# Kernel optimization log

Measured on AMD Instinct MI355X. Metric: run time of the kernel, lower is better.

The kernel has to match this reference:

```python
import jax, jax.numpy as jnp
import numpy as np

N = 100_000       # nodes
E_RAND = 1_600_000
HID = 256         # hidden_channels
L = 4             # num_layers
HEADS = 8
BASES = 4
AGGS = 3          # ['sum','mean','max']
DH = HID // HEADS # 32
BF = DH * BASES   # 128, bases_lin output dim
NG = 5000         # num graphs
VOCAB = 128
NFEAT = 9
EPS = 1e-5


def setup_inputs() -> dict:
    key = jax.random.key(0)
    ks = jax.random.split(key, 16)
    x = jax.random.randint(ks[0], (N, NFEAT), 0, VOCAB, dtype=jnp.int32)
    src = jax.random.randint(ks[1], (E_RAND,), 0, N, dtype=jnp.int32)
    dst = jax.random.randint(ks[2], (E_RAND,), 0, N, dtype=jnp.int32)
    loop = jnp.arange(N, dtype=jnp.int32)          # EGConv add_self_loops=True
    edge_src = jnp.concatenate([src, loop])
    edge_dst = jnp.concatenate([dst, loop])
    batch = jnp.sort(jax.random.randint(ks[3], (N,), 0, NG, dtype=jnp.int32))
    s = lambda k, shape, sc: (jax.random.normal(k, shape, jnp.float32) * sc)
    emb = s(ks[4], (NFEAT, VOCAB, HID), 0.1)       # AtomEncoder tables
    basesW = s(ks[5], (L, HID, BF), HID ** -0.5)
    combW = s(ks[6], (L, HID, HEADS * BASES * AGGS), HID ** -0.5)
    combB = jnp.zeros((L, HEADS * BASES * AGGS), jnp.float32)
    convBias = jnp.zeros((L, HID), jnp.float32)
    bnG = jnp.ones((L, HID), jnp.float32)
    bnB = jnp.zeros((L, HID), jnp.float32)
    mlp_w1 = s(ks[7], (HID, HID // 2), HID ** -0.5)
    bn1_g = jnp.ones((HID // 2,), jnp.float32)
    bn1_b = jnp.zeros((HID // 2,), jnp.float32)
    mlp_w2 = s(ks[8], (HID // 2, HID // 4), (HID // 2) ** -0.5)
    bn2_g = jnp.ones((HID // 4,), jnp.float32)
    bn2_b = jnp.zeros((HID // 4,), jnp.float32)
    mlp_w3 = s(ks[9], (HID // 4, 1), (HID // 4) ** -0.5)
    mlp_b3 = jnp.zeros((1,), jnp.float32)
    return dict(x=x, edge_src=edge_src, edge_dst=edge_dst, batch=batch,
                emb=emb, basesW=basesW, combW=combW, combB=combB,
                convBias=convBias, bnG=bnG, bnB=bnB,
                mlp_w1=mlp_w1, bn1_g=bn1_g, bn1_b=bn1_b,
                mlp_w2=mlp_w2, bn2_g=bn2_g, bn2_b=bn2_b,
                mlp_w3=mlp_w3, mlp_b3=mlp_b3)


def _batchnorm(h, g, b):
    # training-mode BatchNorm1d: biased batch stats
    mu = h.mean(0)
    var = ((h - mu) ** 2).mean(0)
    return (h - mu) * jax.lax.rsqrt(var + EPS) * g + b


def _egconv(x, src, dst, W_b, W_c, b_c, bias):
    bases = x @ W_b                                    # [N, BF]
    w = (x @ W_c + b_c).reshape(N, HEADS, BASES * AGGS)
    msg = bases[src]                                   # [E, BF] gather
    agg_sum = jnp.zeros((N, BF), x.dtype).at[dst].add(msg)
    deg = jnp.zeros((N,), x.dtype).at[dst].add(1.0)
    agg_mean = agg_sum / jnp.maximum(deg, 1.0)[:, None]
    agg_max = jnp.full((N, BF), -jnp.inf, x.dtype).at[dst].max(msg)
    agg = jnp.stack([agg_sum, agg_mean, agg_max], 1)   # [N, A, BF]
    agg = agg.reshape(N, AGGS * BASES, DH)             # [N, A*B, DH]
    out = jnp.einsum('nhk,nkd->nhd', w, agg).reshape(N, HID)
    return out + bias


def reference(x, edge_src, edge_dst, batch, emb, basesW, combW, combB,
              convBias, bnG, bnB, mlp_w1, bn1_g, bn1_b, mlp_w2, bn2_g,
              bn2_b, mlp_w3, mlp_b3):
    # AtomEncoder: sum of per-feature embedding lookups
    h = jnp.take_along_axis(
        emb.transpose(1, 0, 2),                        # [VOCAB, NFEAT, HID]
        x.T[..., None], axis=0) if False else None
    feat = jnp.arange(NFEAT)
    xe = emb[feat[None, :], x, :].sum(1)               # [N, HID]
    h = xe
    for l in range(L):
        c = _egconv(h, edge_src, edge_dst, basesW[l], combW[l], combB[l],
                    convBias[l])
        c = jax.nn.relu(_batchnorm(c, bnG[l], bnB[l]))
        h = h + c                                      # residual
    # global mean pool over graphs
    gs = jax.ops.segment_sum(h, batch, num_segments=NG)
    cnt = jax.ops.segment_sum(jnp.ones((N, 1), h.dtype), batch,
                              num_segments=NG)
    g = gs / jnp.maximum(cnt, 1.0)
    # MLP head
    g = jax.nn.relu(_batchnorm(g @ mlp_w1, bn1_g, bn1_b))
    g = jax.nn.relu(_batchnorm(g @ mlp_w2, bn2_g, bn2_b))
    return g @ mlp_w3 + mlp_b3                         # [NG, 1]
```

## Files before the change

### kernel.cpp

```cpp
#include <hip/hip_runtime.h>
#include <hip/hip_bf16.h>

#define NNODES 100000
#define HIDC 256
#define NFEAT 9
#define VOCABS 128
#define BFD 128
#define NCOMB 96
#define NGR 5000
#define LAYERSN 4
#define EPSV 1e-5f
#define SCHUNK 1024
#define NPP 16
#define NTILES 14
#define AGGBLK 2048
#define AGGW (AGGBLK * 4)
#define PBL (NTILES * 8 * 64)

typedef __hip_bfloat16 bf16;
typedef __attribute__((ext_vector_type(8))) short sh8;
typedef __attribute__((ext_vector_type(4))) float fx4;

__device__ __forceinline__ float b2f(bf16 v) { return __bfloat162float(v); }
__device__ __forceinline__ bf16 f2b(float v) { return __float2bfloat16(v); }
__device__ __forceinline__ float ldf(const float* p) { return *p; }
__device__ __forceinline__ float ldf(const bf16* p) { return b2f(*p); }
__device__ __forceinline__ void stf(float* p, float v) { *p = v; }
__device__ __forceinline__ void stf(bf16* p, float v) { *p = f2b(v); }

__device__ __forceinline__ unsigned pack2bf(float a, float b) {
    unsigned ua = __float_as_uint(a), ub = __float_as_uint(b);
    ua = (ua + 0x7FFFu + ((ua >> 16) & 1u)) >> 16;
    ub = (ub + 0x7FFFu + ((ub >> 16) & 1u)) >> 16;
    return ua | (ub << 16);
}

__global__ __launch_bounds__(256) void k_sentinel(float* out, int n, float val) {
    int i = blockIdx.x * 256 + threadIdx.x;
    if (i < n) out[i] = val;
}

template <typename TH>
__global__ __launch_bounds__(256) void k_atom(const int* __restrict__ x,
                                              const float* __restrict__ emb,
                                              TH* __restrict__ h) {
    int n = blockIdx.x;
    __shared__ int xs[NFEAT];
    if (threadIdx.x < NFEAT) xs[threadIdx.x] = x[n * NFEAT + threadIdx.x];
    __syncthreads();
    int c = threadIdx.x;
    float acc = 0.f;
#pragma unroll
    for (int f = 0; f < NFEAT; ++f)
        acc += emb[(f * VOCABS + xs[f]) * HIDC + c];
    stf(&h[(size_t)n * HIDC + c], acc);
}

__global__ __launch_bounds__(256) void k_hist(const int* __restrict__ dst,
                                              int* __restrict__ counts, int E) {
    int e = blockIdx.x * 256 + threadIdx.x;
    if (e < E) atomicAdd(&counts[dst[e]], 1);
}

__global__ __launch_bounds__(256) void k_scansum(const int* __restrict__ counts,
                                                 int* __restrict__ btot, int n) {
    __shared__ int sh[256];
    int b = blockIdx.x, t = threadIdx.x;
    int base = b * SCHUNK;
    int s = 0;
#pragma unroll
    for (int k = 0; k < 4; ++k) {
        int i = base + t + k * 256;
        if (i < n) s += counts[i];
    }
    sh[t] = s;
    __syncthreads();
    for (int st = 128; st > 0; st >>= 1) {
        if (t < st) sh[t] += sh[t + st];
        __syncthreads();
    }
    if (t == 0) btot[b] = sh[0];
}

__global__ void k_scansmall(const int* __restrict__ btot, int* __restrict__ boff, int nb) {
    if (threadIdx.x == 0 && blockIdx.x == 0) {
        int a = 0;
        for (int i = 0; i < nb; ++i) { boff[i] = a; a += btot[i]; }
    }
}

__global__ __launch_bounds__(256) void k_scanapply(const int* __restrict__ counts,
                                                   const int* __restrict__ boff,
                                                   int* __restrict__ rowptr,
                                                   int* __restrict__ cursor, int n) {
    __shared__ int sh[256];
    int b = blockIdx.x, t = threadIdx.x;
    int base = b * SCHUNK + t * 4;
    int c0 = (base + 0 < n) ? counts[base + 0] : 0;
    int c1 = (base + 1 < n) ? counts[base + 1] : 0;
    int c2 = (base + 2 < n) ? counts[base + 2] : 0;
    int c3 = (base + 3 < n) ? counts[base + 3] : 0;
    int s0 = c0, s1 = s0 + c1, s2 = s1 + c2, s3 = s2 + c3;
    sh[t] = s3;
    __syncthreads();
    for (int st = 1; st < 256; st <<= 1) {
        int v = (t >= st) ? sh[t - st] : 0;
        __syncthreads();
        sh[t] += v;
        __syncthreads();
    }
    int excl = sh[t] - s3 + boff[b];
    if (base + 0 < n) { rowptr[base + 1] = excl + s0; cursor[base + 0] = excl; }
    if (base + 1 < n) { rowptr[base + 2] = excl + s1; cursor[base + 1] = excl + s0; }
    if (base + 2 < n) { rowptr[base + 3] = excl + s2; cursor[base + 2] = excl + s1; }
    if (base + 3 < n) { rowptr[base + 4] = excl + s3; cursor[base + 3] = excl + s2; }
    if (b == 0 && t == 0) rowptr[0] = 0;
}

__global__ __launch_bounds__(256) void k_scatter(const int* __restrict__ src,
                                                 const int* __restrict__ dst,
                                                 int* __restrict__ cursor,
                                                 int* __restrict__ csr, int E) {
    int e = blockIdx.x * 256 + threadIdx.x;
    if (e >= E) return;
    int pos = atomicAdd(&cursor[dst[e]], 1);
    csr[pos] = src[e];
}

__global__ __launch_bounds__(256) void k_packB4(const float* __restrict__ basesW,
                                                const float* __restrict__ combW,
                                                bf16* __restrict__ Bp4) {
    int tid = blockIdx.x * 256 + threadIdx.x;
    if (tid >= LAYERSN * PBL) return;
    int layer = tid / PBL;
    int rem = tid % PBL;
    int l = rem & 63;
    int q = (rem >> 6) & 7;
    int t = rem >> 9;
    int n = t * 16 + (l & 15);
    int k0 = q * 32 + (l >> 4) * 8;
    const float* Wb = basesW + (size_t)layer * HIDC * BFD;
    const float* Wc = combW + (size_t)layer * HIDC * NCOMB;
    short out[8];
#pragma unroll
    for (int i = 0; i < 8; ++i) {
        int k = k0 + i;
        float v = (n < BFD) ? Wb[k * BFD + n] : Wc[k * NCOMB + (n - BFD)];
        unsigned u = __float_as_uint(v);
        out[i] = (short)((u + 0x7FFFu + ((u >> 16) & 1u)) >> 16);
    }
    *(sh8*)(Bp4 + (size_t)tid * 8) = *(sh8*)out;
}

template <typename TH, typename TW>
__global__ __launch_bounds__(256) void k_gemm_mfma(TH* __restrict__ h,
                                                   const bf16* __restrict__ Bp,
                                                   const float* __restrict__ cb,
                                                   bf16* __restrict__ bases,
                                                   TW* __restrict__ wco,
                                                   const bf16* __restrict__ convp,
                                                   const float* __restrict__ ss) {
    __shared__ unsigned ldsA[8192];
    int tid = threadIdx.x;
    size_t blk = blockIdx.x;
#pragma unroll 4
    for (int it = 0; it < 32; ++it) {
        int p = tid + it * 256;
        int row = p >> 7, cp = p & 127;
        size_t rg = blk * 64 + row;
        unsigned word = 0;
        if (rg < NNODES) {
            int c0 = cp * 2;
            float a0 = ldf(&h[rg * HIDC + c0]);
            float a1 = ldf(&h[rg * HIDC + c0 + 1]);
            if (convp) {
                float v0 = b2f(convp[rg * HIDC + c0]) * ss[c0] + ss[HIDC + c0];
                float v1 = b2f(convp[rg * HIDC + c0 + 1]) * ss[c0 + 1] + ss[HIDC + c0 + 1];
                a0 += fmaxf(v0, 0.f);
                a1 += fmaxf(v1, 0.f);
                stf(&h[rg * HIDC + c0], a0);
                stf(&h[rg * HIDC + c0 + 1], a1);
            }
            word = pack2bf(a0, a1);
        }
        ldsA[(row * 128 + cp) ^ ((row & 7) << 2)] = word;
    }
    __syncthreads();
    int w = tid >> 6, l = tid & 63;
    int r = 16 * w + (l & 15);
    sh8 af[8];
    const char* lb = (const char*)ldsA;
#pragma unroll
    for (int q = 0; q < 8; ++q) {
        int byte = (r * 512 + q * 64 + (l >> 4) * 16) ^ ((r & 7) << 4);
        af[q] = *(const sh8*)(lb + byte);
    }
    fx4 acc[NTILES];
#pragma unroll
    for (int t = 0; t < NTILES; ++t) acc[t] = (fx4){0.f, 0.f, 0.f, 0.f};
    const sh8* bp8 = (const sh8*)Bp;
#pragma unroll
    for (int t = 0; t < NTILES; ++t) {
#pragma unroll
        for (int q = 0; q < 8; ++q) {
            acc[t] = __builtin_amdgcn_mfma_f32_16x16x32_bf16(
                af[q], bp8[(t * 8 + q) * 64 + l], acc[t], 0, 0, 0);
        }
    }
#pragma unroll
    for (int t = 0; t < NTILES; ++t) {
#pragma unroll
        for (int j = 0; j < 4; ++j) {
            int rl = 16 * w + (l >> 4) * 4 + j;
            size_t rg = blk * 64 + rl;
            if (rg >= NNODES) continue;
            if (t < 8) {
                int col = t * 16 + (l & 15);
                bases[rg * BFD + col] = f2b(acc[t][j]);
            } else {
                int col = (t - 8) * 16 + (l & 15);
                stf(&wco[rg * NCOMB + col], acc[t][j] + cb[col]);
            }
        }
    }
}

template <typename TW>
__global__ __launch_bounds__(256) void k_agg(const int* __restrict__ rowptr,
                                             const int* __restrict__ csr,
                                             const uint2* __restrict__ b2,
                                             const TW* __restrict__ wco,
                                             const float* __restrict__ bias,
                                             bf16* __restrict__ conv,
                                             float* __restrict__ partials) {
    __shared__ float agg[4][3][BFD];
    __shared__ int nid[4];
    int tid = threadIdx.x;
    int wv = tid >> 6, lane = tid & 63;
    int cl = lane & 31;
    bool loh = lane < 32;
    int c = tid, hh = c >> 5, d = c & 31;
    float bb = bias[c];
    float st_s = 0.f, st_s2 = 0.f;
    const int ITERS = (NNODES + AGGW - 1) / AGGW;
    int n = blockIdx.x * 4 + wv;
    for (int it = 0; it < ITERS; ++it, n += AGGW) {
        if (n < NNODES) {
            if (lane == 0) nid[wv] = n;
            int r0 = rowptr[n], r1 = rowptr[n + 1];
            float s0 = 0.f, s1 = 0.f, s2 = 0.f, s3 = 0.f;
            float m0 = -INFINITY, m1 = -INFINITY, m2 = -INFINITY, m3 = -INFINITY;
            int e = r0;
#define ACCU2(v) { float f0 = __uint_as_float((v).x << 16);            \
                   float f1 = __uint_as_float((v).x & 0xFFFF0000u);    \
                   float f2 = __uint_as_float((v).y << 16);            \
                   float f3 = __uint_as_float((v).y & 0xFFFF0000u);    \
                   s0 += f0; s1 += f1; s2 += f2; s3 += f3;             \
                   m0 = fmaxf(m0, f0); m1 = fmaxf(m1, f1);             \
                   m2 = fmaxf(m2, f2); m3 = fmaxf(m3, f3); }
            for (; e + 4 <= r1; e += 4) {
                int sa = loh ? csr[e + 0] : csr[e + 1];
                int sb = loh ? csr[e + 2] : csr[e + 3];
                uint2 va = b2[(size_t)sa * 32 + cl];
                uint2 vb = b2[(size_t)sb * 32 + cl];
                ACCU2(va) ACCU2(vb)
            }
            for (; e + 2 <= r1; e += 2) {
                int sa = loh ? csr[e + 0] : csr[e + 1];
                uint2 va = b2[(size_t)sa * 32 + cl];
                ACCU2(va)
            }
            if (e < r1 && loh) {
                uint2 va = b2[(size_t)csr[e] * 32 + cl];
                ACCU2(va)
            }
#undef ACCU2
            float t0 = s0 + __shfl_xor(s0, 32);
            float t1 = s1 + __shfl_xor(s1, 32);
            float t2 = s2 + __shfl_xor(s2, 32);
            float t3 = s3 + __shfl_xor(s3, 32);
            float x0 = fmaxf(m0, __shfl_xor(m0, 32));
            float x1 = fmaxf(m1, __shfl_xor(m1, 32));
            float x2 = fmaxf(m2, __shfl_xor(m2, 32));
            float x3 = fmaxf(m3, __shfl_xor(m3, 32));
            if (loh) {
                float inv = 1.0f / (float)(r1 - r0);
                int cc = 4 * cl;
                agg[wv][0][cc + 0] = t0; agg[wv][1][cc + 0] = t0 * inv; agg[wv][2][cc + 0] = x0;
                agg[wv][0][cc + 1] = t1; agg[wv][1][cc + 1] = t1 * inv; agg[wv][2][cc + 1] = x1;
                agg[wv][0][cc + 2] = t2; agg[wv][1][cc + 2] = t2 * inv; agg[wv][2][cc + 2] = x2;
                agg[wv][0][cc + 3] = t3; agg[wv][1][cc + 3] = t3 * inv; agg[wv][2][cc + 3] = x3;
            }
        } else if (lane == 0) {
            nid[wv] = -1;
        }
        __syncthreads();
#pragma unroll
        for (int w2 = 0; w2 < 4; ++w2) {
            int n2 = nid[w2];
            if (n2 < 0) continue;
            const TW* wp = &wco[(size_t)n2 * NCOMB + hh * 12];
            float a = 0.f;
#pragma unroll
            for (int b = 0; b < 4; ++b) {
                a += ldf(&wp[0 + b]) * agg[w2][0][b * 32 + d];
                a += ldf(&wp[4 + b]) * agg[w2][1][b * 32 + d];
                a += ldf(&wp[8 + b]) * agg[w2][2][b * 32 + d];
            }
            a += bb;
            conv[(size_t)n2 * HIDC + c] = f2b(a);
            st_s += a;
            st_s2 += a * a;
        }
        __syncthreads();
    }
    partials[(size_t)blockIdx.x * 512 + c] = st_s;
    partials[(size_t)blockIdx.x * 512 + 256 + c] = st_s2;
}

__global__ __launch_bounds__(256) void k_redstats(const float* __restrict__ partials,
                                                  float* __restrict__ sums) {
    int g = blockIdx.x * 256 + threadIdx.x;
    int j = g & 511;
    int chunk = g >> 9;
    float s = 0.f;
    for (int pb = chunk * 256; pb < (chunk + 1) * 256; ++pb)
        s += partials[(size_t)pb * 512 + j];
    atomicAdd(&sums[j], s);
}

template <int C>
__global__ void k_bnfin(const float* __restrict__ sums, const float* __restrict__ g,
                        const float* __restrict__ b, float nrows, float* __restrict__ ss) {
    int c = threadIdx.x;
    float mu = sums[c] / nrows;
    float var = sums[C + c] / nrows - mu * mu;
    float rstd = rsqrtf(fmaxf(var, 0.f) + EPSV);
    float sc = rstd * g[c];
    ss[c] = sc;
    ss[C + c] = b[c] - mu * sc;
}

template <typename TH>
__global__ __launch_bounds__(256) void k_apply_res(const bf16* __restrict__ conv,
                                                   const float* __restrict__ ss,
                                                   TH* __restrict__ h) {
    int n = blockIdx.x;
    int c = threadIdx.x;
    float v = b2f(conv[(size_t)n * HIDC + c]) * ss[c] + ss[HIDC + c];
    size_t i = (size_t)n * HIDC + c;
    stf(&h[i], ldf(&h[i]) + fmaxf(v, 0.f));
}

template <typename TH>
__global__ __launch_bounds__(256) void k_pool(const TH* __restrict__ h,
                                              const int* __restrict__ batch,
                                              float* __restrict__ gs,
                                              float* __restrict__ cnt) {
    int c = threadIdx.x;
    int n0 = blockIdx.x * NPP;
    int end = min(n0 + NPP, NNODES);
    float acc = 0.f, ccnt = 0.f;
    int cur = batch[n0];
    for (int n = n0; n < end; ++n) {
        int b = batch[n];
        if (b != cur) {
            atomicAdd(&gs[(size_t)cur * HIDC + c], acc);
            if (c == 0) atomicAdd(&cnt[cur], ccnt);
            acc = 0.f; ccnt = 0.f; cur = b;
        }
        acc += ldf(&h[(size_t)n * HIDC + c]);
        ccnt += 1.f;
    }
    atomicAdd(&gs[(size_t)cur * HIDC + c], acc);
    if (c == 0) atomicAdd(&cnt[cur], ccnt);
}

__global__ __launch_bounds__(256) void k_pooldiv(float* __restrict__ gs,
                                                 const float* __restrict__ cnt) {
    int i = blockIdx.x * 256 + threadIdx.x;
    if (i >= NGR * HIDC) return;
    int ng = i >> 8;
    gs[i] = gs[i] / fmaxf(cnt[ng], 1.0f);
}

template <int K, int C>
__global__ void k_rowgemm(const float* __restrict__ in, const float* __restrict__ W,
                          float* __restrict__ out) {
    int r = blockIdx.x;
    __shared__ float rs[K];
    for (int i = threadIdx.x; i < K; i += C) rs[i] = in[r * K + i];
    __syncthreads();
    int c = threadIdx.x;
    float acc = 0.f;
    for (int k = 0; k < K; ++k) acc += rs[k] * W[k * C + c];
    out[r * C + c] = acc;
}

template <int C>
__global__ void k_stats(const float* __restrict__ a, int rows, int rpb,
                        float* __restrict__ sums) {
    int c = threadIdx.x;
    int r0 = blockIdx.x * rpb;
    int r1 = min(r0 + rpb, rows);
    float s = 0.f, s2 = 0.f;
    for (int r = r0; r < r1; ++r) {
        float v = a[r * C + c];
        s += v;
        s2 += v * v;
    }
    atomicAdd(&sums[c], s);
    atomicAdd(&sums[C + c], s2);
}

template <int C>
__global__ void k_apply_relu(float* __restrict__ a, const float* __restrict__ ss, int rows) {
    int i = blockIdx.x * 256 + threadIdx.x;
    if (i >= rows * C) return;
    int c = i % C;
    float v = a[i] * ss[c] + ss[C + c];
    a[i] = fmaxf(v, 0.f);
}

__global__ __launch_bounds__(256) void k_final(const float* __restrict__ g2,
                                               const float* __restrict__ w3,
                                               const float* __restrict__ b3,
                                               float* __restrict__ out) {
    int r = blockIdx.x * 256 + threadIdx.x;
    if (r >= NGR) return;
    float acc = 0.f;
#pragma unroll
    for (int k = 0; k < 64; ++k) acc += g2[r * 64 + k] * w3[k];
    out[r] = acc + b3[0];
}

static inline size_t alignup(size_t v) { return (v + 255) & ~(size_t)255; }

template <typename TH, typename TW>
static size_t carve_need(int E) {
    size_t off = 0;
    off = alignup(off + (size_t)NNODES * HIDC * sizeof(TH));
    off = alignup(off + (size_t)NNODES * BFD * 2);
    off = alignup(off + (size_t)NNODES * NCOMB * sizeof(TW));
    off = alignup(off + (size_t)NNODES * HIDC * 2);
    off = alignup(off + (size_t)(NNODES + 1) * 4);
    off = alignup(off + (size_t)NNODES * 4);
    off = alignup(off + (size_t)E * 4);
    off = alignup(off + 2 * HIDC * 4);
    off = alignup(off + 2 * HIDC * 4);
    off = alignup(off + 256 * 4);
    off = alignup(off + 256 * 4);
    off = alignup(off + (size_t)LAYERSN * PBL * 8 * 2);
    off = alignup(off + (size_t)AGGBLK * 512 * 4);
    return off;
}

template <typename TH, typename TW>
static void run_all(const int* x, const int* esrc, const int* edst, const int* batch,
                    const float* emb, const float* basesW, const float* combW,
                    const float* combB, const float* convB, const float* bnG,
                    const float* bnB, const float* w1, const float* bn1g,
                    const float* bn1b, const float* w2, const float* bn2g,
                    const float* bn2b, const float* w3, const float* b3, int E,
                    float* out, char* base, hipStream_t stream) {
    size_t off = 0;
    TH* h = (TH*)(base + off);       off = alignup(off + (size_t)NNODES * HIDC * sizeof(TH));
    bf16* bases = (bf16*)(base + off); off = alignup(off + (size_t)NNODES * BFD * 2);
    TW* wco = (TW*)(base + off);     off = alignup(off + (size_t)NNODES * NCOMB * sizeof(TW));
    size_t o_conv = off;
    bf16* conv = (bf16*)(base + off); off = alignup(off + (size_t)NNODES * HIDC * 2);
    int* rowptr = (int*)(base + off); off = alignup(off + (size_t)(NNODES + 1) * 4);
    int* cursor = (int*)(base + off); off = alignup(off + (size_t)NNODES * 4);
    int* csr = (int*)(base + off);    off = alignup(off + (size_t)E * 4);
    float* sums = (float*)(base + off); off = alignup(off + 2 * HIDC * 4);
    float* ss = (float*)(base + off);   off = alignup(off + 2 * HIDC * 4);
    int* btot = (int*)(base + off);     off = alignup(off + 256 * 4);
    int* boff = (int*)(base + off);     off = alignup(off + 256 * 4);
    bf16* Bp4 = (bf16*)(base + off);    off = alignup(off + (size_t)LAYERSN * PBL * 8 * 2);
    float* partials = (float*)(base + off); off = alignup(off + (size_t)AGGBLK * 512 * 4);
    size_t po = o_conv;
    float* gs = (float*)(base + po);  po = alignup(po + (size_t)NGR * HIDC * 4);
    float* cnt = (float*)(base + po); po = alignup(po + (size_t)NGR * 4);
    float* r1 = (float*)(base + po);  po = alignup(po + (size_t)NGR * 128 * 4);
    float* r2 = (float*)(base + po);  po = alignup(po + (size_t)NGR * 64 * 4);

    const int NB = (NNODES + SCHUNK - 1) / SCHUNK;
    const int GEMMBLK = (NNODES + 63) / 64;

    k_atom<TH><<<NNODES, 256, 0, stream>>>(x, emb, h);
    k_packB4<<<(LAYERSN * PBL + 255) / 256, 256, 0, stream>>>(basesW, combW, Bp4);
    hipMemsetAsync(cursor, 0, (size_t)NNODES * 4, stream);
    k_hist<<<(E + 255) / 256, 256, 0, stream>>>(edst, cursor, E);
    k_scansum<<<NB, 256, 0, stream>>>(cursor, btot, NNODES);
    k_scansmall<<<1, 64, 0, stream>>>(btot, boff, NB);
    k_scanapply<<<NB, 256, 0, stream>>>(cursor, boff, rowptr, cursor, NNODES);
    k_scatter<<<(E + 255) / 256, 256, 0, stream>>>(esrc, edst, cursor, csr, E);

    for (int l = 0; l < LAYERSN; ++l) {
        hipMemsetAsync(sums, 0, 2 * HIDC * 4, stream);
        k_gemm_mfma<TH, TW><<<GEMMBLK, 256, 0, stream>>>(
            h, Bp4 + (size_t)l * PBL * 8, combB + (size_t)l * NCOMB, bases, wco,
            (l > 0) ? conv : (const bf16*)nullptr, ss);
        k_agg<TW><<<AGGBLK, 256, 0, stream>>>(rowptr, csr, (const uint2*)bases,
                                              wco, convB + (size_t)l * HIDC, conv,
                                              partials);
        k_redstats<<<16, 256, 0, stream>>>(partials, sums);
        k_bnfin<HIDC><<<1, HIDC, 0, stream>>>(sums, bnG + (size_t)l * HIDC,
                                              bnB + (size_t)l * HIDC, (float)NNODES, ss);
    }
    k_apply_res<TH><<<NNODES, 256, 0, stream>>>(conv, ss, h);

    hipMemsetAsync(gs, 0, (size_t)NGR * HIDC * 4, stream);
    hipMemsetAsync(cnt, 0, (size_t)NGR * 4, stream);
    k_pool<TH><<<(NNODES + NPP - 1) / NPP, 256, 0, stream>>>(h, batch, gs, cnt);
    k_pooldiv<<<(NGR * HIDC + 255) / 256, 256, 0, stream>>>(gs, cnt);

    k_rowgemm<256, 128><<<NGR, 128, 0, stream>>>(gs, w1, r1);
    hipMemsetAsync(sums, 0, 2 * 128 * 4, stream);
    k_stats<128><<<(NGR + 15) / 16, 128, 0, stream>>>(r1, NGR, 16, sums);
    k_bnfin<128><<<1, 128, 0, stream>>>(sums, bn1g, bn1b, (float)NGR, ss);
    k_apply_relu<128><<<(NGR * 128 + 255) / 256, 256, 0, stream>>>(r1, ss, NGR);

    k_rowgemm<128, 64><<<NGR, 64, 0, stream>>>(r1, w2, r2);
    hipMemsetAsync(sums, 0, 2 * 64 * 4, stream);
    k_stats<64><<<(NGR + 31) / 32, 64, 0, stream>>>(r2, NGR, 32, sums);
    k_bnfin<64><<<1, 64, 0, stream>>>(sums, bn2g, bn2b, (float)NGR, ss);
    k_apply_relu<64><<<(NGR * 64 + 255) / 256, 256, 0, stream>>>(r2, ss, NGR);

    k_final<<<(NGR + 255) / 256, 256, 0, stream>>>(r2, w3, b3, out);
}

extern "C" void kernel_launch(void* const* d_in, const int* in_sizes, int n_in,
                              void* d_out, int out_size, void* d_ws, size_t ws_size,
                              hipStream_t stream) {
    const int* x        = (const int*)d_in[0];
    const int* esrc     = (const int*)d_in[1];
    const int* edst     = (const int*)d_in[2];
    const int* batch    = (const int*)d_in[3];
    const float* emb    = (const float*)d_in[4];
    const float* basesW = (const float*)d_in[5];
    const float* combW  = (const float*)d_in[6];
    const float* combB  = (const float*)d_in[7];
    const float* convB  = (const float*)d_in[8];
    const float* bnG    = (const float*)d_in[9];
    const float* bnB    = (const float*)d_in[10];
    const float* w1     = (const float*)d_in[11];
    const float* bn1g   = (const float*)d_in[12];
    const float* bn1b   = (const float*)d_in[13];
    const float* w2     = (const float*)d_in[14];
    const float* bn2g   = (const float*)d_in[15];
    const float* bn2b   = (const float*)d_in[16];
    const float* w3     = (const float*)d_in[17];
    const float* b3     = (const float*)d_in[18];
    const int E = in_sizes[1];

    size_t need_full    = carve_need<float, float>(E);
    size_t need_compact = carve_need<bf16, bf16>(E);

    if (ws_size >= need_full) {
        run_all<float, float>(x, esrc, edst, batch, emb, basesW, combW, combB, convB,
                              bnG, bnB, w1, bn1g, bn1b, w2, bn2g, bn2b, w3, b3, E,
                              (float*)d_out, (char*)d_ws, stream);
    } else if (ws_size >= need_compact) {
        run_all<bf16, bf16>(x, esrc, edst, batch, emb, basesW, combW, combB, convB,
                            bnG, bnB, w1, bn1g, bn1b, w2, bn2g, bn2b, w3, b3, E,
                            (float*)d_out, (char*)d_ws, stream);
    } else {
        k_sentinel<<<(out_size + 255) / 256, 256, 0, stream>>>(
            (float*)d_out, out_size, (float)(ws_size >> 20));
    }
}
```

Before: 1.499 ms.

## Bucket edges by destination before CSR scatter and drop block sync in aggregation

The CSR build now runs in two passes. Edges are first partitioned into 32 destination-range buckets using block-local counts, then each bucket is scattered by its own group of blocks, so the atomics and csr writes hit a narrower address range. The aggregation kernel now has each wavefront apply the per-node combination weights to its own node, with each lane producing 4 packed bf16 channels. This removes the per-iteration __syncthreads and the shared node-id exchange. BN statistics are reduced through shared-memory atomics, at the cost of an extra edge buffer and more kernel launches.

```diff
diff --git a/kernel.cpp b/kernel.cpp
--- a/kernel.cpp
+++ b/kernel.cpp
@@ -16,6 +16,9 @@
 #define AGGBLK 2048
 #define AGGW (AGGBLK * 4)
 #define PBL (NTILES * 8 * 64)
+#define NBUK 32
+#define BDIV 3125
+#define SC2K 16
 
 typedef __hip_bfloat16 bf16;
 typedef __attribute__((ext_vector_type(8))) short sh8;
@@ -117,14 +120,56 @@
     if (b == 0 && t == 0) rowptr[0] = 0;
 }
 
-__global__ __launch_bounds__(256) void k_scatter(const int* __restrict__ src,
-                                                 const int* __restrict__ dst,
-                                                 int* __restrict__ cursor,
-                                                 int* __restrict__ csr, int E) {
-    int e = blockIdx.x * 256 + threadIdx.x;
-    if (e >= E) return;
-    int pos = atomicAdd(&cursor[dst[e]], 1);
-    csr[pos] = src[e];
+__global__ void k_binit(const int* __restrict__ rowptr, int* __restrict__ gcur) {
+    int b = threadIdx.x;
+    if (b < NBUK) gcur[b] = rowptr[b * BDIV];
+}
+
+__global__ __launch_bounds__(256) void k_bucket(const int* __restrict__ src,
+                                                const int* __restrict__ dst,
+                                                int* __restrict__ gcur,
+                                                uint2* __restrict__ ebuf, int E) {
+    __shared__ int cnt[NBUK], base[NBUK], off[NBUK];
+    int tid = threadIdx.x;
+    if (tid < NBUK) { cnt[tid] = 0; off[tid] = 0; }
+    __syncthreads();
+    int d[4], s[4], bk[4];
+    int e0 = blockIdx.x * 1024;
+#pragma unroll
+    for (int k = 0; k < 4; ++k) {
+        int e = e0 + tid + k * 256;
+        if (e < E) {
+            d[k] = dst[e]; s[k] = src[e];
+            bk[k] = d[k] / BDIV;
+            atomicAdd(&cnt[bk[k]], 1);
+        } else bk[k] = -1;
+    }
+    __syncthreads();
+    if (tid < NBUK && cnt[tid] > 0) base[tid] = atomicAdd(&gcur[tid], cnt[tid]);
+    __syncthreads();
+#pragma unroll
+    for (int k = 0; k < 4; ++k) {
+        if (bk[k] >= 0) {
+            int sl = base[bk[k]] + atomicAdd(&off[bk[k]], 1);
+            ebuf[sl] = make_uint2((unsigned)d[k], (unsigned)s[k]);
+        }
+    }
+}
+
+__global__ __launch_bounds__(256) void k_scatter2(const uint2* __restrict__ ebuf,
+                                                  const int* __restrict__ rowptr,
+                                                  int* __restrict__ cursor,
+                                                  int* __restrict__ csr) {
+    int bk = blockIdx.x & (NBUK - 1);
+    int chunk = blockIdx.x >> 5;
+    int lo = rowptr[bk * BDIV];
+    int nhi = (bk + 1) * BDIV; if (nhi > NNODES) nhi = NNODES;
+    int hi = rowptr[nhi];
+    for (int e = lo + chunk * 256 + threadIdx.x; e < hi; e += SC2K * 256) {
+        uint2 p = ebuf[e];
+        int pos = atomicAdd(&cursor[p.x], 1);
+        csr[pos] = (int)p.y;
+    }
 }
 
 __global__ __launch_bounds__(256) void k_packB4(const float* __restrict__ basesW,
@@ -234,23 +279,24 @@
                                              bf16* __restrict__ conv,
                                              float* __restrict__ partials) {
     __shared__ float agg[4][3][BFD];
-    __shared__ int nid[4];
+    __shared__ float red[512];
     int tid = threadIdx.x;
     int wv = tid >> 6, lane = tid & 63;
     int cl = lane & 31;
     bool loh = lane < 32;
-    int c = tid, hh = c >> 5, d = c & 31;
-    float bb = bias[c];
-    float st_s = 0.f, st_s2 = 0.f;
-    const int ITERS = (NNODES + AGGW - 1) / AGGW;
-    int n = blockIdx.x * 4 + wv;
-    for (int it = 0; it < ITERS; ++it, n += AGGW) {
-        if (n < NNODES) {
-            if (lane == 0) nid[wv] = n;
-            int r0 = rowptr[n], r1 = rowptr[n + 1];
-            float s0 = 0.f, s1 = 0.f, s2 = 0.f, s3 = 0.f;
-            float m0 = -INFINITY, m1 = -INFINITY, m2 = -INFINITY, m3 = -INFINITY;
-            int e = r0;
+    red[tid] = 0.f;
+    red[tid + 256] = 0.f;
+    __syncthreads();
+    int hh = lane >> 3;
+    float bb[4];
+#pragma unroll
+    for (int j = 0; j < 4; ++j) bb[j] = bias[4 * lane + j];
+    float sts[4] = {0.f, 0.f, 0.f, 0.f}, sts2[4] = {0.f, 0.f, 0.f, 0.f};
+    for (int n = blockIdx.x * 4 + wv; n < NNODES; n += AGGW) {
+        int r0 = rowptr[n], r1 = rowptr[n + 1];
+        float s0 = 0.f, s1 = 0.f, s2 = 0.f, s3 = 0.f;
+        float m0 = -INFINITY, m1 = -INFINITY, m2 = -INFINITY, m3 = -INFINITY;
+        int e = r0;
 #define ACCU2(v) { float f0 = __uint_as_float((v).x << 16);            \
                    float f1 = __uint_as_float((v).x & 0xFFFF0000u);    \
                    float f2 = __uint_as_float((v).y << 16);            \
@@ -258,64 +304,70 @@
                    s0 += f0; s1 += f1; s2 += f2; s3 += f3;             \
                    m0 = fmaxf(m0, f0); m1 = fmaxf(m1, f1);             \
                    m2 = fmaxf(m2, f2); m3 = fmaxf(m3, f3); }
-            for (; e + 4 <= r1; e += 4) {
-                int sa = loh ? csr[e + 0] : csr[e + 1];
-                int sb = loh ? csr[e + 2] : csr[e + 3];
-                uint2 va = b2[(size_t)sa * 32 + cl];
-                uint2 vb = b2[(size_t)sb * 32 + cl];
-                ACCU2(va) ACCU2(vb)
+        for (; e + 4 <= r1; e += 4) {
+            int sa = loh ? csr[e + 0] : csr[e + 1];
+            int sb = loh ? csr[e + 2] : csr[e + 3];
+            uint2 va = b2[(size_t)sa * 32 + cl];
+            uint2 vb = b2[(size_t)sb * 32 + cl];
+            ACCU2(va) ACCU2(vb)
+        }
+        for (; e + 2 <= r1; e += 2) {
+            int sa = loh ? csr[e + 0] : csr[e + 1];
+            uint2 va = b2[(size_t)sa * 32 + cl];
+            ACCU2(va)
+        }
+        if (e < r1 && loh) {
+            uint2 va = b2[(size_t)csr[e] * 32 + cl];
+            ACCU2(va)
+        }
+#undef ACCU2
+        float t0 = s0 + __shfl_xor(s0, 32);
+        float t1 = s1 + __shfl_xor(s1, 32);
+        float t2 = s2 + __shfl_xor(s2, 32);
+        float t3 = s3 + __shfl_xor(s3, 32);
+        float x0 = fmaxf(m0, __shfl_xor(m0, 32));
+        float x1 = fmaxf(m1, __shfl_xor(m1, 32));
+        float x2 = fmaxf(m2, __shfl_xor(m2, 32));
+        float x3 = fmaxf(m3, __shfl_xor(m3, 32));
+        if (loh) {
+            float inv = 1.0f / (float)(r1 - r0);
+            int cc = 4 * cl;
+            agg[wv][0][cc + 0] = t0; agg[wv][1][cc + 0] = t0 * inv; agg[wv][2][cc + 0] = x0;
+            agg[wv][0][cc + 1] = t1; agg[wv][1][cc + 1] = t1 * inv; agg[wv][2][cc + 1] = x1;
+            agg[wv][0][cc + 2] = t2; agg[wv][1][cc + 2] = t2 * inv; agg[wv][2][cc + 2] = x2;
+            agg[wv][0][cc + 3] = t3; agg[wv][1][cc + 3] = t3 * inv; agg[wv][2][cc + 3] = x3;
+        }
+        const TW* wp = &wco[(size_t)n * NCOMB + hh * 12];
+        float w[12];
+#pragma unroll
+        for (int k = 0; k < 12; ++k) w[k] = ldf(&wp[k]);
+        float o[4];
+#pragma unroll
+        for (int j = 0; j < 4; ++j) {
+            int d = (4 * lane + j) & 31;
+            float a = 0.f;
+#pragma unroll
+            for (int b = 0; b < 4; ++b) {
+                a += w[b] * agg[wv][0][b * 32 + d];
+                a += w[4 + b] * agg[wv][1][b * 32 + d];
+                a += w[8 + b] * agg[wv][2][b * 32 + d];
             }
-            for (; e + 2 <= r1; e += 2) {
-                int sa = loh ? csr[e + 0] : csr[e + 1];
-                uint2 va = b2[(size_t)sa * 32 + cl];
-                ACCU2(va)
-            }
-            if (e < r1 && loh) {
-                uint2 va = b2[(size_t)csr[e] * 32 + cl];
-                ACCU2(va)
-            }
-#undef ACCU2
-            float t0 = s0 + __shfl_xor(s0, 32);
-            float t1 = s1 + __shfl_xor(s1, 32);
-            float t2 = s2 + __shfl_xor(s2, 32);
-            float t3 = s3 + __shfl_xor(s3, 32);
-            float x0 = fmaxf(m0, __shfl_xor(m0, 32));
-            float x1 = fmaxf(m1, __shfl_xor(m1, 32));
-            float x2 = fmaxf(m2, __shfl_xor(m2, 32));
-            float x3 = fmaxf(m3, __shfl_xor(m3, 32));
-            if (loh) {
-                float inv = 1.0f / (float)(r1 - r0);
-                int cc = 4 * cl;
-                agg[wv][0][cc + 0] = t0; agg[wv][1][cc + 0] = t0 * inv; agg[wv][2][cc + 0] = x0;
-                agg[wv][0][cc + 1] = t1; agg[wv][1][cc + 1] = t1 * inv; agg[wv][2][cc + 1] = x1;
-                agg[wv][0][cc + 2] = t2; agg[wv][1][cc + 2] = t2 * inv; agg[wv][2][cc + 2] = x2;
-                agg[wv][0][cc + 3] = t3; agg[wv][1][cc + 3] = t3 * inv; agg[wv][2][cc + 3] = x3;
-            }
-        } else if (lane == 0) {
-            nid[wv] = -1;
-        }
-        __syncthreads();
-#pragma unroll
-        for (int w2 = 0; w2 < 4; ++w2) {
-            int n2 = nid[w2];
-            if (n2 < 0) continue;
-            const TW* wp = &wco[(size_t)n2 * NCOMB + hh * 12];
-            float a = 0.f;
-#pragma unroll
-            for (int b = 0; b < 4; ++b) {
-                a += ldf(&wp[0 + b]) * agg[w2][0][b * 32 + d];
-                a += ldf(&wp[4 + b]) * agg[w2][1][b * 32 + d];
-                a += ldf(&wp[8 + b]) * agg[w2][2][b * 32 + d];
-            }
-            a += bb;
-            conv[(size_t)n2 * HIDC + c] = f2b(a);
-            st_s += a;
-            st_s2 += a * a;
-        }
-        __syncthreads();
-    }
-    partials[(size_t)blockIdx.x * 512 + c] = st_s;
-    partials[(size_t)blockIdx.x * 512 + 256 + c] = st_s2;
+            a += bb[j];
+            o[j] = a;
+            sts[j] += a;
+            sts2[j] += a * a;
+        }
+        uint2 cv = make_uint2(pack2bf(o[0], o[1]), pack2bf(o[2], o[3]));
+        ((uint2*)conv)[(size_t)n * 64 + lane] = cv;
+    }
+#pragma unroll
+    for (int j = 0; j < 4; ++j) {
+        atomicAdd(&red[4 * lane + j], sts[j]);
+        atomicAdd(&red[256 + 4 * lane + j], sts2[j]);
+    }
+    __syncthreads();
+    partials[(size_t)blockIdx.x * 512 + tid] = red[tid];
+    partials[(size_t)blockIdx.x * 512 + 256 + tid] = red[tid + 256];
 }
 
 __global__ __launch_bounds__(256) void k_redstats(const float* __restrict__ partials,
@@ -446,8 +498,10 @@
     off = alignup(off + (size_t)(NNODES + 1) * 4);
     off = alignup(off + (size_t)NNODES * 4);
     off = alignup(off + (size_t)E * 4);
+    off = alignup(off + (size_t)E * 8);
     off = alignup(off + 2 * HIDC * 4);
     off = alignup(off + 2 * HIDC * 4);
+    off = alignup(off + 256 * 4);
     off = alignup(off + 256 * 4);
     off = alignup(off + 256 * 4);
     off = alignup(off + (size_t)LAYERSN * PBL * 8 * 2);
@@ -472,10 +526,12 @@
     int* rowptr = (int*)(base + off); off = alignup(off + (size_t)(NNODES + 1) * 4);
     int* cursor = (int*)(base + off); off = alignup(off + (size_t)NNODES * 4);
     int* csr = (int*)(base + off);    off = alignup(off + (size_t)E * 4);
+    uint2* ebuf = (uint2*)(base + off); off = alignup(off + (size_t)E * 8);
     float* sums = (float*)(base + off); off = alignup(off + 2 * HIDC * 4);
     float* ss = (float*)(base + off);   off = alignup(off + 2 * HIDC * 4);
     int* btot = (int*)(base + off);     off = alignup(off + 256 * 4);
     int* boff = (int*)(base + off);     off = alignup(off + 256 * 4);
+    int* gcur = (int*)(base + off);     off = alignup(off + 256 * 4);
     bf16* Bp4 = (bf16*)(base + off);    off = alignup(off + (size_t)LAYERSN * PBL * 8 * 2);
     float* partials = (float*)(base + off); off = alignup(off + (size_t)AGGBLK * 512 * 4);
     size_t po = o_conv;
@@ -494,7 +550,9 @@
     k_scansum<<<NB, 256, 0, stream>>>(cursor, btot, NNODES);
     k_scansmall<<<1, 64, 0, stream>>>(btot, boff, NB);
     k_scanapply<<<NB, 256, 0, stream>>>(cursor, boff, rowptr, cursor, NNODES);
-    k_scatter<<<(E + 255) / 256, 256, 0, stream>>>(esrc, edst, cursor, csr, E);
+    k_binit<<<1, NBUK, 0, stream>>>(rowptr, gcur);
+    k_bucket<<<(E + 1023) / 1024, 256, 0, stream>>>(esrc, edst, gcur, ebuf, E);
+    k_scatter2<<<NBUK * SC2K, 256, 0, stream>>>(ebuf, rowptr, cursor, csr);
 
     for (int l = 0; l < LAYERSN; ++l) {
         hipMemsetAsync(sums, 0, 2 * HIDC * 4, stream);
```

After: 1.579 ms. +5.3%, slower.
